# Optimization experiments

Hardware: AMD Instinct MI355X
Metric: run time of the kernel (lower is better)

Reference implementation:

```python
import jax, jax.numpy as jnp
import numpy as np

B, N, C, H = 2, 2048, 1024, 16
D = C // H  # head_dim = 64


def setup_inputs() -> dict:
    key = jax.random.key(0)
    ks = jax.random.split(key, 5)
    s = 1.0 / np.sqrt(C)
    return {
        "q": jax.random.normal(ks[0], (B, N, C), dtype=jnp.float32),
        "W_qkv": jax.random.normal(ks[1], (C, 3 * C), dtype=jnp.float32) * s,
        "b_qkv": jnp.zeros((3 * C,), dtype=jnp.float32),
        "W_proj": jax.random.normal(ks[2], (C, C), dtype=jnp.float32) * s,
        "b_proj": jnp.zeros((C,), dtype=jnp.float32),
    }


def reference(q, W_qkv, b_qkv, W_proj, b_proj):
    # Self-attention: k = v = q. Full 3C projection (as in the torch code).
    qkv = q @ W_qkv + b_qkv  # [B, N, 3C]
    qh = qkv[:, :, :C].reshape(B, N, H, D)
    kh = qkv[:, :, C:2 * C].reshape(B, N, H, D)
    vh = qkv[:, :, 2 * C:].reshape(B, N, H, D)
    scale = D ** -0.5
    # [B, H, N, N] attention logits
    attn = jnp.einsum("bnhd,bmhd->bhnm", qh, kh) * scale
    attn = jax.nn.softmax(attn, axis=-1)
    out = jnp.einsum("bhnm,bmhd->bnhd", attn, vh).reshape(B, N, C)
    return out @ W_proj + b_proj
```

## Files before the change

### kernel.cpp

```cpp
#include <hip/hip_runtime.h>
#include <stdint.h>

typedef __bf16 bf16_t;
typedef __bf16 bf16x8 __attribute__((ext_vector_type(8)));
typedef __bf16 bf16x4 __attribute__((ext_vector_type(4)));
typedef float f32x4 __attribute__((ext_vector_type(4)));

#define L2E 1.44269504088896340736f
#define QSCALE (0.125f * L2E)

__device__ __forceinline__ void gload16(const bf16_t* g, bf16_t* l) {
  __builtin_amdgcn_global_load_lds(
      (const __attribute__((address_space(1))) void*)g,
      (__attribute__((address_space(3))) void*)l, 16, 0, 0);
}

__global__ __launch_bounds__(256) void cast_q_kernel(const float* __restrict__ in,
                                                     bf16_t* __restrict__ out) {
  int i = blockIdx.x * 256 + threadIdx.x;
  float4 v = reinterpret_cast<const float4*>(in)[i];
  bf16x4 o;
  o[0] = (bf16_t)v.x; o[1] = (bf16_t)v.y; o[2] = (bf16_t)v.z; o[3] = (bf16_t)v.w;
  reinterpret_cast<bf16x4*>(out)[i] = o;
}

__global__ __launch_bounds__(256) void transpose_cast_kernel(const float* __restrict__ in,
                                                             bf16_t* __restrict__ out,
                                                             int K, int N) {
  __shared__ float tile[64][65];
  int k0 = blockIdx.y * 64, n0 = blockIdx.x * 64;
  int t = threadIdx.x;
  int r = t >> 4, c4 = (t & 15) * 4;
#pragma unroll
  for (int rr = 0; rr < 4; rr++) {
    int row = r + rr * 16;
    float4 v = *reinterpret_cast<const float4*>(&in[(size_t)(k0 + row) * N + n0 + c4]);
    tile[row][c4 + 0] = v.x; tile[row][c4 + 1] = v.y;
    tile[row][c4 + 2] = v.z; tile[row][c4 + 3] = v.w;
  }
  __syncthreads();
#pragma unroll
  for (int rr = 0; rr < 4; rr++) {
    int nr = r + rr * 16;
    bf16x4 o;
#pragma unroll
    for (int i = 0; i < 4; i++) o[i] = (bf16_t)tile[c4 + i][nr];
    *reinterpret_cast<bf16x4*>(&out[(size_t)(n0 + nr) * K + k0 + c4]) = o;
  }
}

template <int MODE>
__global__ __launch_bounds__(256) void gemm_kernel(const bf16_t* __restrict__ A,
                                                   const bf16_t* __restrict__ Bt,
                                                   const float* __restrict__ bias,
                                                   void* __restrict__ out,
                                                   bf16_t* __restrict__ vT,
                                                   int K, int gm, int gn, int ldo) {
  __shared__ __align__(16) bf16_t smem[17408];
  bf16_t* At = smem;
  bf16_t* Bts = smem + 8192;
  const int t = threadIdx.x, lane = t & 63, w = t >> 6;
  const int g = lane >> 4, q = lane & 15;
  const int bid = blockIdx.x, x = bid & 7, r = bid >> 3;
  const int qm = gm >> 2, qn = gn >> 1;
  const int lm = r % qm, ln = r / qm;
  const int m0 = ((x & 3) * qm + lm) * 128, n0 = ((x >> 2) * qn + ln) * 128;
  const int wm = (w >> 1) * 64, wn = (w & 1) * 64;

  const bf16_t* srcA[4]; const bf16_t* srcB[4]; int dsto[4];
#pragma unroll
  for (int i = 0; i < 4; i++) {
    int gI = i * 256 + t;
    int row = gI >> 3, p = (gI & 7) ^ (row & 7);
    srcA[i] = A + (size_t)(m0 + row) * K + p * 8;
    srcB[i] = Bt + (size_t)(n0 + row) * K + p * 8;
    dsto[i] = (i * 256 + w * 64) * 8;
  }

  f32x4 acc[4][4];
#pragma unroll
  for (int i = 0; i < 4; i++)
#pragma unroll
    for (int j = 0; j < 4; j++) acc[i][j] = (f32x4){0.f, 0.f, 0.f, 0.f};

  for (int k0 = 0; k0 < K; k0 += 64) {
    __syncthreads();
#pragma unroll
    for (int i = 0; i < 4; i++) {
      gload16(srcA[i] + k0, &At[dsto[i]]);
      gload16(srcB[i] + k0, &Bts[dsto[i]]);
    }
    __syncthreads();
#pragma unroll
    for (int dc = 0; dc < 2; dc++) {
      bf16x8 am[4], bn[4];
#pragma unroll
      for (int i = 0; i < 4; i++) {
        int ra = wm + 16 * i + q;
        am[i] = *reinterpret_cast<const bf16x8*>(&At[ra * 64 + ((dc * 32 + g * 8) ^ ((ra & 7) * 8))]);
        int rb = wn + 16 * i + q;
        bn[i] = *reinterpret_cast<const bf16x8*>(&Bts[rb * 64 + ((dc * 32 + g * 8) ^ ((rb & 7) * 8))]);
      }
      __builtin_amdgcn_s_setprio(1);
#pragma unroll
      for (int i = 0; i < 4; i++)
#pragma unroll
        for (int j = 0; j < 4; j++)
          acc[i][j] = __builtin_amdgcn_mfma_f32_16x16x32_bf16(am[i], bn[j], acc[i][j], 0, 0, 0);
      __builtin_amdgcn_s_setprio(0);
    }
  }

  if (MODE == 0 && n0 >= 2048) {
    __syncthreads();
    bf16_t* TT = smem;
#pragma unroll
    for (int i = 0; i < 4; i++)
#pragma unroll
      for (int j = 0; j < 4; j++)
#pragma unroll
        for (int rr = 0; rr < 4; rr++) {
          int ch = wn + 16 * j + q;
          int tok = wm + 16 * i + 4 * g + rr;
          float v = acc[i][j][rr] + bias[n0 + ch];
          TT[ch * 136 + (((tok >> 3) ^ (ch & 7)) * 8) + (tok & 7)] = (bf16_t)v;
        }
    __syncthreads();
    const int bb = m0 >> 11;
    const int t0 = m0 & 2047;
#pragma unroll
    for (int it = 0; it < 8; it++) {
      int ch = it * 16 + w * 4 + (lane >> 4);
      int ck = lane & 15;
      uint4 val = *reinterpret_cast<const uint4*>(&TT[ch * 136 + ((ck ^ (ch & 7)) * 8)]);
      int vch = (n0 - 2048) + ch;
      bf16_t* dst = vT + ((size_t)(bb * 16 + (vch >> 6)) * 64 + (vch & 63)) * 2048 + t0 + ck * 8;
      *reinterpret_cast<uint4*>(dst) = val;
    }
  } else {
#pragma unroll
    for (int i = 0; i < 4; i++)
#pragma unroll
      for (int j = 0; j < 4; j++)
#pragma unroll
        for (int rr = 0; rr < 4; rr++) {
          int row = m0 + wm + 16 * i + 4 * g + rr;
          int col = n0 + wn + 16 * j + q;
          float v = acc[i][j][rr] + bias[col];
          if (MODE == 0) {
            if (col < 1024) v *= QSCALE;
            ((bf16_t*)out)[(size_t)row * ldo + col] = (bf16_t)v;
          } else {
            ((float*)out)[(size_t)row * ldo + col] = v;
          }
        }
  }
}

__global__ __launch_bounds__(256) void attn_kernel(const bf16_t* __restrict__ qk,
                                                   const bf16_t* __restrict__ vT,
                                                   bf16_t* __restrict__ aout) {
  __shared__ __align__(16) bf16_t sK[2][4096];
  __shared__ __align__(16) bf16_t sV[2][4096];
  __shared__ __align__(16) bf16_t sP[4][1024];

  const int t = threadIdx.x, lane = t & 63, w = t >> 6;
  const int g = lane >> 4, q = lane & 15;
  const int bid = blockIdx.x, xr = bid >> 3;
  const int bh = (bid & 7) * 4 + (xr >> 5);
  const int b = bh >> 4, h = bh & 15;
  const int q0 = (xr & 31) * 64 + w * 16;
  const bf16_t* qk_b = qk + (size_t)b * 2048 * 2048;
  const bf16_t* vT_h = vT + (size_t)bh * 64 * 2048;
  bf16_t* Pw = sP[w];

  const bf16_t* srcK[2]; const bf16_t* srcV[2]; int dsto[2];
#pragma unroll
  for (int i = 0; i < 2; i++) {
    int gI = (w * 2 + i) * 64 + lane;
    int row = gI >> 3, p = (gI & 7) ^ (row & 7);
    srcK[i] = qk_b + (size_t)row * 2048 + 1024 + h * 64 + p * 8;
    srcV[i] = vT_h + (size_t)row * 2048 + p * 8;
    dsto[i] = (w * 2 + i) * 512;
  }

  bf16x8 bq[2];
  {
    const bf16_t* qr = qk_b + (size_t)(q0 + q) * 2048 + h * 64;
    bq[0] = *reinterpret_cast<const bf16x8*>(qr + g * 8);
    bq[1] = *reinterpret_cast<const bf16x8*>(qr + 32 + g * 8);
  }

  bf16x8 ones;
#pragma unroll
  for (int i = 0; i < 8; i++) ones[i] = (bf16_t)1.0f;

  f32x4 oacc[4];
#pragma unroll
  for (int c = 0; c < 4; c++) oacc[c] = (f32x4){0.f, 0.f, 0.f, 0.f};
  f32x4 lacc = (f32x4){0.f, 0.f, 0.f, 0.f};

#pragma unroll
  for (int i = 0; i < 2; i++) {
    gload16(srcK[i], &sK[0][dsto[i]]);
    gload16(srcV[i], &sV[0][dsto[i]]);
  }
  __syncthreads();

  for (int tt = 0; tt < 32; tt++) {
    const int cur = tt & 1;
    if (tt + 1 < 32) {
      size_t koffK = (size_t)(tt + 1) * 64 * 2048;
      size_t koffV = (size_t)(tt + 1) * 64;
#pragma unroll
      for (int i = 0; i < 2; i++) {
        gload16(srcK[i] + koffK, &sK[cur ^ 1][dsto[i]]);
        gload16(srcV[i] + koffV, &sV[cur ^ 1][dsto[i]]);
      }
    }

    const bf16_t* Kc = sK[cur];
    f32x4 s[4];
    __builtin_amdgcn_s_setprio(1);
#pragma unroll
    for (int c = 0; c < 4; c++) {
      int row = 16 * c + q, sw = (q & 7) * 8;
      bf16x8 ka0 = *reinterpret_cast<const bf16x8*>(&Kc[row * 64 + ((g * 8) ^ sw)]);
      bf16x8 ka1 = *reinterpret_cast<const bf16x8*>(&Kc[row * 64 + ((32 + g * 8) ^ sw)]);
      f32x4 z = (f32x4){0.f, 0.f, 0.f, 0.f};
      z = __builtin_amdgcn_mfma_f32_16x16x32_bf16(ka0, bq[0], z, 0, 0, 0);
      z = __builtin_amdgcn_mfma_f32_16x16x32_bf16(ka1, bq[1], z, 0, 0, 0);
      s[c] = z;
    }
    __builtin_amdgcn_s_setprio(0);

#pragma unroll
    for (int c = 0; c < 4; c++) {
      bf16x4 pk;
#pragma unroll
      for (int rr = 0; rr < 4; rr++) pk[rr] = (bf16_t)exp2f(s[c][rr]);
      *reinterpret_cast<bf16x4*>(
          &Pw[q * 64 + (((2 * c + (g >> 1)) ^ (q & 7)) * 8) + (g & 1) * 4]) = pk;
    }

    const bf16_t* Vc = sV[cur];
    __builtin_amdgcn_s_setprio(1);
#pragma unroll
    for (int kc = 0; kc < 2; kc++) {
      bf16x8 pb = *reinterpret_cast<const bf16x8*>(
          &Pw[q * 64 + (((kc * 4 + g) ^ (q & 7)) * 8)]);
      lacc = __builtin_amdgcn_mfma_f32_16x16x32_bf16(ones, pb, lacc, 0, 0, 0);
#pragma unroll
      for (int c = 0; c < 4; c++) {
        int row = 16 * c + q;
        bf16x8 va = *reinterpret_cast<const bf16x8*>(
            &Vc[row * 64 + (((kc * 4 + g) ^ (q & 7)) * 8)]);
        oacc[c] = __builtin_amdgcn_mfma_f32_16x16x32_bf16(va, pb, oacc[c], 0, 0, 0);
      }
    }
    __builtin_amdgcn_s_setprio(0);

    __syncthreads();
  }

  float inv = 1.0f / lacc[0];
  bf16_t* orow = aout + (size_t)(b * 2048 + q0 + q) * 1024 + h * 64;
#pragma unroll
  for (int c = 0; c < 4; c++) {
    bf16x4 ov;
#pragma unroll
    for (int rr = 0; rr < 4; rr++) ov[rr] = (bf16_t)(oacc[c][rr] * inv);
    *reinterpret_cast<bf16x4*>(orow + c * 16 + g * 4) = ov;
  }
}

extern "C" void kernel_launch(void* const* d_in, const int* in_sizes, int n_in,
                              void* d_out, int out_size, void* d_ws, size_t ws_size,
                              hipStream_t stream) {
  const float* q     = (const float*)d_in[0];
  const float* Wqkv  = (const float*)d_in[1];
  const float* bqkv  = (const float*)d_in[2];
  const float* Wproj = (const float*)d_in[3];
  const float* bproj = (const float*)d_in[4];
  float* out = (float*)d_out;

  char* ws = (char*)d_ws;
  bf16_t* q_bf    = (bf16_t*)(ws);
  bf16_t* wqkv_t  = (bf16_t*)(ws + 8388608);
  bf16_t* wproj_t = (bf16_t*)(ws + 14680064);
  bf16_t* qk      = (bf16_t*)(ws + 16777216);
  bf16_t* vT      = (bf16_t*)(ws + 33554432);
  bf16_t* aout    = q_bf;

  cast_q_kernel<<<4096, 256, 0, stream>>>(q, q_bf);
  transpose_cast_kernel<<<dim3(48, 16), 256, 0, stream>>>(Wqkv, wqkv_t, 1024, 3072);
  transpose_cast_kernel<<<dim3(16, 16), 256, 0, stream>>>(Wproj, wproj_t, 1024, 1024);
  gemm_kernel<0><<<768, 256, 0, stream>>>(q_bf, wqkv_t, bqkv, qk, vT, 1024, 32, 24, 2048);
  attn_kernel<<<1024, 256, 0, stream>>>(qk, vT, aout);
  gemm_kernel<1><<<256, 256, 0, stream>>>(aout, wproj_t, bproj, out, nullptr, 1024, 32, 8, 1024);
}
```

Baseline: 149.4 us.

## Halve proj GEMM M-tile, drop setprio hints, use raw v_exp_f32 in attention

The GEMM kernel is templated on the M tile size, and the output projection now uses 64-row tiles over 512 blocks instead of 256, so more CUs are busy on the small projection GEMM. The per-thread global-to-LDS load mapping is reworked into a unified chunk loop that covers both A and B. All s_setprio priority hints are removed from the GEMM and attention kernels. The attention exp2 now uses an inline v_exp_f32, skipping exp2f's range handling, which is acceptable given the scaled logits.

After: 134.5 us. 10.0% less time.

```diff
diff --git a/kernel.cpp b/kernel.cpp
--- a/kernel.cpp
+++ b/kernel.cpp
@@ -13,6 +13,12 @@
   __builtin_amdgcn_global_load_lds(
       (const __attribute__((address_space(1))) void*)g,
       (__attribute__((address_space(3))) void*)l, 16, 0, 0);
+}
+
+__device__ __forceinline__ float fexp2(float x) {
+  float r;
+  asm("v_exp_f32 %0, %1" : "=v"(r) : "v"(x));
+  return r;
 }
 
 __global__ __launch_bounds__(256) void cast_q_kernel(const float* __restrict__ in,
@@ -49,65 +55,69 @@
   }
 }
 
-template <int MODE>
+template <int MODE, int BM>
 __global__ __launch_bounds__(256) void gemm_kernel(const bf16_t* __restrict__ A,
                                                    const bf16_t* __restrict__ Bt,
                                                    const float* __restrict__ bias,
                                                    void* __restrict__ out,
                                                    bf16_t* __restrict__ vT,
                                                    int K, int gm, int gn, int ldo) {
-  __shared__ __align__(16) bf16_t smem[17408];
+  constexpr int ACH = BM / 8;
+  constexpr int NCH = ACH + 16;
+  constexpr int CPW = NCH / 4;
+  constexpr int IR = BM / 32;
+  constexpr int SMEM = (MODE == 0) ? 17408 : (BM * 64 + 8192);
+  __shared__ __align__(16) bf16_t smem[SMEM];
   bf16_t* At = smem;
-  bf16_t* Bts = smem + 8192;
+  bf16_t* Bts = smem + BM * 64;
   const int t = threadIdx.x, lane = t & 63, w = t >> 6;
   const int g = lane >> 4, q = lane & 15;
   const int bid = blockIdx.x, x = bid & 7, r = bid >> 3;
   const int qm = gm >> 2, qn = gn >> 1;
   const int lm = r % qm, ln = r / qm;
-  const int m0 = ((x & 3) * qm + lm) * 128, n0 = ((x >> 2) * qn + ln) * 128;
-  const int wm = (w >> 1) * 64, wn = (w & 1) * 64;
-
-  const bf16_t* srcA[4]; const bf16_t* srcB[4]; int dsto[4];
-#pragma unroll
-  for (int i = 0; i < 4; i++) {
-    int gI = i * 256 + t;
-    int row = gI >> 3, p = (gI & 7) ^ (row & 7);
-    srcA[i] = A + (size_t)(m0 + row) * K + p * 8;
-    srcB[i] = Bt + (size_t)(n0 + row) * K + p * 8;
-    dsto[i] = (i * 256 + w * 64) * 8;
-  }
-
-  f32x4 acc[4][4];
-#pragma unroll
-  for (int i = 0; i < 4; i++)
+  const int m0 = ((x & 3) * qm + lm) * BM, n0 = ((x >> 2) * qn + ln) * 128;
+  const int wm = (w >> 1) * (BM / 2), wn = (w & 1) * 64;
+
+  const bf16_t* srcp[CPW]; int dsto[CPW];
+#pragma unroll
+  for (int i = 0; i < CPW; i++) {
+    int cI = i * 4 + w;
+    bool isA = cI < ACH;
+    int row = (isA ? cI : cI - ACH) * 8 + (lane >> 3);
+    int p = (lane & 7) ^ (row & 7);
+    srcp[i] = (isA ? A + (size_t)(m0 + row) * K : Bt + (size_t)(n0 + row) * K) + p * 8;
+    dsto[i] = (isA ? cI * 512 : BM * 64 + (cI - ACH) * 512);
+  }
+
+  f32x4 acc[IR][4];
+#pragma unroll
+  for (int i = 0; i < IR; i++)
 #pragma unroll
     for (int j = 0; j < 4; j++) acc[i][j] = (f32x4){0.f, 0.f, 0.f, 0.f};
 
   for (int k0 = 0; k0 < K; k0 += 64) {
     __syncthreads();
 #pragma unroll
-    for (int i = 0; i < 4; i++) {
-      gload16(srcA[i] + k0, &At[dsto[i]]);
-      gload16(srcB[i] + k0, &Bts[dsto[i]]);
-    }
+    for (int i = 0; i < CPW; i++) gload16(srcp[i] + k0, &smem[dsto[i]]);
     __syncthreads();
 #pragma unroll
     for (int dc = 0; dc < 2; dc++) {
-      bf16x8 am[4], bn[4];
-#pragma unroll
-      for (int i = 0; i < 4; i++) {
+      bf16x8 am[IR], bn[4];
+#pragma unroll
+      for (int i = 0; i < IR; i++) {
         int ra = wm + 16 * i + q;
         am[i] = *reinterpret_cast<const bf16x8*>(&At[ra * 64 + ((dc * 32 + g * 8) ^ ((ra & 7) * 8))]);
-        int rb = wn + 16 * i + q;
-        bn[i] = *reinterpret_cast<const bf16x8*>(&Bts[rb * 64 + ((dc * 32 + g * 8) ^ ((rb & 7) * 8))]);
       }
-      __builtin_amdgcn_s_setprio(1);
-#pragma unroll
-      for (int i = 0; i < 4; i++)
+#pragma unroll
+      for (int j = 0; j < 4; j++) {
+        int rb = wn + 16 * j + q;
+        bn[j] = *reinterpret_cast<const bf16x8*>(&Bts[rb * 64 + ((dc * 32 + g * 8) ^ ((rb & 7) * 8))]);
+      }
+#pragma unroll
+      for (int i = 0; i < IR; i++)
 #pragma unroll
         for (int j = 0; j < 4; j++)
           acc[i][j] = __builtin_amdgcn_mfma_f32_16x16x32_bf16(am[i], bn[j], acc[i][j], 0, 0, 0);
-      __builtin_amdgcn_s_setprio(0);
     }
   }
 
@@ -115,7 +125,7 @@
     __syncthreads();
     bf16_t* TT = smem;
 #pragma unroll
-    for (int i = 0; i < 4; i++)
+    for (int i = 0; i < IR; i++)
 #pragma unroll
       for (int j = 0; j < 4; j++)
 #pragma unroll
@@ -139,7 +149,7 @@
     }
   } else {
 #pragma unroll
-    for (int i = 0; i < 4; i++)
+    for (int i = 0; i < IR; i++)
 #pragma unroll
       for (int j = 0; j < 4; j++)
 #pragma unroll
@@ -221,7 +231,6 @@
 
     const bf16_t* Kc = sK[cur];
     f32x4 s[4];
-    __builtin_amdgcn_s_setprio(1);
 #pragma unroll
     for (int c = 0; c < 4; c++) {
       int row = 16 * c + q, sw = (q & 7) * 8;
@@ -232,19 +241,17 @@
       z = __builtin_amdgcn_mfma_f32_16x16x32_bf16(ka1, bq[1], z, 0, 0, 0);
       s[c] = z;
     }
-    __builtin_amdgcn_s_setprio(0);
 
 #pragma unroll
     for (int c = 0; c < 4; c++) {
       bf16x4 pk;
 #pragma unroll
-      for (int rr = 0; rr < 4; rr++) pk[rr] = (bf16_t)exp2f(s[c][rr]);
+      for (int rr = 0; rr < 4; rr++) pk[rr] = (bf16_t)fexp2(s[c][rr]);
       *reinterpret_cast<bf16x4*>(
           &Pw[q * 64 + (((2 * c + (g >> 1)) ^ (q & 7)) * 8) + (g & 1) * 4]) = pk;
     }
 
     const bf16_t* Vc = sV[cur];
-    __builtin_amdgcn_s_setprio(1);
 #pragma unroll
     for (int kc = 0; kc < 2; kc++) {
       bf16x8 pb = *reinterpret_cast<const bf16x8*>(
@@ -258,7 +265,6 @@
         oacc[c] = __builtin_amdgcn_mfma_f32_16x16x32_bf16(va, pb, oacc[c], 0, 0, 0);
       }
     }
-    __builtin_amdgcn_s_setprio(0);
 
     __syncthreads();
   }
@@ -295,7 +301,7 @@
   cast_q_kernel<<<4096, 256, 0, stream>>>(q, q_bf);
   transpose_cast_kernel<<<dim3(48, 16), 256, 0, stream>>>(Wqkv, wqkv_t, 1024, 3072);
   transpose_cast_kernel<<<dim3(16, 16), 256, 0, stream>>>(Wproj, wproj_t, 1024, 1024);
-  gemm_kernel<0><<<768, 256, 0, stream>>>(q_bf, wqkv_t, bqkv, qk, vT, 1024, 32, 24, 2048);
+  gemm_kernel<0, 128><<<768, 256, 0, stream>>>(q_bf, wqkv_t, bqkv, qk, vT, 1024, 32, 24, 2048);
   attn_kernel<<<1024, 256, 0, stream>>>(qk, vT, aout);
-  gemm_kernel<1><<<256, 256, 0, stream>>>(aout, wproj_t, bproj, out, nullptr, 1024, 32, 8, 1024);
-}
+  gemm_kernel<1, 64><<<512, 256, 0, stream>>>(aout, wproj_t, bproj, out, nullptr, 1024, 64, 8, 1024);
+}
```
